# Performance work log

Hardware: AMD Instinct MI355X
Metric: run time of the kernel (lower is better)

The kernel has to match this reference:

```python
import jax, jax.numpy as jnp
import numpy as np

NMS_THRESH = 0.5
SCORE_THRESH = 0.2
MAX_SUBJECT = 15
MAX_OBJECT = 15
B, NS, NO = 32, 512, 512


def _make_boxes(k, b, n):
    u = jax.random.uniform(k, (b, n, 4))
    xy = u[..., :2] * 1000.0          # top-left corner
    wh = u[..., 2:] * 200.0 + 1.0     # positive width/height
    return jnp.concatenate([xy, xy + wh], axis=-1)  # valid xyxy boxes


def setup_inputs() -> dict:
    key = jax.random.key(0)
    ks = jax.random.split(key, 6)
    return {
        "subj_boxes": _make_boxes(ks[0], B, NS),
        "subj_scores": jax.random.uniform(ks[1], (B, NS)),
        "subj_labels": jax.random.randint(ks[2], (B, NS), 0, 30, dtype=jnp.int32),
        "obj_boxes": _make_boxes(ks[3], B, NO),
        "obj_scores": jax.random.uniform(ks[4], (B, NO)),
        "obj_labels": jax.random.randint(ks[5], (B, NO), 0, 30, dtype=jnp.int32),
    }


def reference(subj_boxes, subj_scores, subj_labels, obj_boxes, obj_scores, obj_labels):
    # concat subject + object detections per image, as in preprocess()
    boxes = jnp.concatenate([subj_boxes, obj_boxes], axis=1)    # [B,N,4]
    scores = jnp.concatenate([subj_scores, obj_scores], axis=1) # [B,N]
    labels = jnp.concatenate([subj_labels, obj_labels], axis=1) # [B,N]
    b, n = scores.shape
    is_subj = jnp.arange(n) < subj_boxes.shape[1]               # [N]

    # sort by score descending (matches the argsort after NMS; greedy NMS
    # preserves this ordering among survivors)
    order = jnp.argsort(-scores, axis=1)
    boxes = jnp.take_along_axis(boxes, order[..., None], axis=1)
    scores = jnp.take_along_axis(scores, order, axis=1)
    labels = jnp.take_along_axis(labels, order, axis=1)
    is_subj = jnp.take(is_subj, order)                          # [B,N]

    active = scores >= SCORE_THRESH

    # torchvision batched_nms: offset boxes per class so distinct classes
    # never overlap (comparisons only -> no gradient path)
    max_coord = jax.lax.stop_gradient(jnp.max(boxes))
    ob = boxes + labels.astype(boxes.dtype)[..., None] * (max_coord + 1.0)

    # pairwise IoU [B,N,N]
    area = (ob[..., 2] - ob[..., 0]) * (ob[..., 3] - ob[..., 1])
    lt = jnp.maximum(ob[:, :, None, :2], ob[:, None, :, :2])
    rb = jnp.minimum(ob[:, :, None, 2:], ob[:, None, :, 2:])
    wh = jnp.clip(rb - lt, 0.0)
    inter = wh[..., 0] * wh[..., 1]
    iou = inter / (area[:, :, None] + area[:, None, :] - inter)

    later = jnp.arange(n)[None, :] > jnp.arange(n)[:, None]     # strictly lower-score

    def body(i, suppressed):  # greedy NMS, vectorized over batch
        keep_i = active[:, i] & ~suppressed[:, i]
        return suppressed | (keep_i[:, None] & (iou[:, i, :] > NMS_THRESH) & later[i])

    suppressed = jax.lax.fori_loop(0, n, body, jnp.zeros((b, n), dtype=bool))
    kept = active & ~suppressed

    # split survivors into subjects / objects, keep top max_subject/max_object
    neg = jnp.finfo(scores.dtype).min
    sub_key = jnp.where(kept & is_subj, scores, neg)
    obj_key = jnp.where(kept & ~is_subj, scores, neg)
    sv, si = jax.lax.top_k(sub_key, MAX_SUBJECT)
    ov, oi = jax.lax.top_k(obj_key, MAX_OBJECT)
    idx = jnp.concatenate([si, oi], axis=1)                     # [B,K]
    valid = jnp.concatenate([sv, ov], axis=1) > neg             # [B,K]

    out_boxes = jnp.take_along_axis(boxes, idx[..., None], axis=1) * valid[..., None]
    out_scores = jnp.take_along_axis(scores, idx, axis=1) * valid
    out_labels = jnp.where(valid, jnp.take_along_axis(labels, idx, axis=1), -1)
    num_subjects = jnp.sum(sv > neg, axis=1)
    return out_boxes, out_scores, out_labels, num_subjects, valid
```

## Files before the change

### kernel.cpp

```cpp
#include <hip/hip_runtime.h>
#include <stdint.h>

#define BQ    32
#define NSUB  512
#define NDET  1024
#define NCLS  30
#define KSLOT 30
#define BCAP  96

#pragma clang fp contract(off)

typedef unsigned long long u64;

__global__ __launch_bounds__(512) void bucket_kernel(
    const float* __restrict__ sb, const float* __restrict__ ss,
    const int*   __restrict__ sl,
    const float* __restrict__ ob, const float* __restrict__ os,
    const int*   __restrict__ ol,
    float* __restrict__ pmax, int* __restrict__ cnts,
    u64* __restrict__ bkeys)
{
    const int b    = blockIdx.x;
    const int t    = threadIdx.x;
    const int lane = t & 63;
    const int w    = t >> 6;

    __shared__ int   lcnt[NCLS];
    __shared__ u64   lkey[NCLS][BCAP];
    __shared__ float wred[8];

    if (t < NCLS) lcnt[t] = 0;

    const float4* s4 = (const float4*)(sb + (size_t)b * NSUB * 4);
    const float4* o4 = (const float4*)(ob + (size_t)b * NSUB * 4);
    float4 a = s4[t], c4 = o4[t];
    float m = fmaxf(fmaxf(fmaxf(a.x, a.y), fmaxf(a.z, a.w)),
                    fmaxf(fmaxf(c4.x, c4.y), fmaxf(c4.z, c4.w)));
    for (int off = 32; off; off >>= 1) m = fmaxf(m, __shfl_xor(m, off));
    if (lane == 0) wred[w] = m;
    __syncthreads();
    if (t == 0) {
        float mm = wred[0];
        for (int i = 1; i < 8; ++i) mm = fmaxf(mm, wred[i]);
        pmax[b] = mm;
    }

    {
        float sc = ss[b * NSUB + t];
        int   lb = sl[b * NSUB + t];
        if (sc >= 0.2f) {
            int pos = atomicAdd(&lcnt[lb], 1);
            if (pos < BCAP)
                lkey[lb][pos] = ((u64)__float_as_uint(sc) << 32) | (u64)(1023 - t);
        }
    }
    {
        float sc = os[b * NSUB + t];
        int   lb = ol[b * NSUB + t];
        if (sc >= 0.2f) {
            int pos = atomicAdd(&lcnt[lb], 1);
            if (pos < BCAP)
                lkey[lb][pos] = ((u64)__float_as_uint(sc) << 32) | (u64)(1023 - (512 + t));
        }
    }
    __syncthreads();

    if (t < NCLS) {
        int c = lcnt[t];
        cnts[b * NCLS + t] = (c < BCAP) ? c : BCAP;
    }
    for (int s = t; s < NCLS * BCAP; s += 512) {
        int c = s / BCAP, k = s - c * BCAP;
        if (k < lcnt[c])
            bkeys[((size_t)b * NCLS + c) * BCAP + k] = lkey[c][k];
    }
}

__global__ __launch_bounds__(64) void nms_class_kernel(
    const float* __restrict__ sb, const float* __restrict__ ob,
    const float* __restrict__ pmax, const int* __restrict__ cnts,
    const u64* __restrict__ bkeys,
    u64* __restrict__ subk, u64* __restrict__ objk)
{
#pragma clang fp contract(off)
    const int c    = blockIdx.x;
    const int b    = blockIdx.y;
    const int lane = threadIdx.x;

    __shared__ u64    keyarr[BCAP];
    __shared__ u64    skey[BCAP];
    __shared__ float4 bx4[BCAP];

    float pv = pmax[lane & 31];
    for (int off = 32; off; off >>= 1) pv = fmaxf(pv, __shfl_xor(pv, off));
    const float mco  = pv + 1.0f;
    const float offc = (float)c * mco;

    int cnt = cnts[b * NCLS + c];
    const u64* src = bkeys + ((size_t)b * NCLS + c) * BCAP;
    if (lane < cnt)        keyarr[lane]      = src[lane];
    if (64 + lane < cnt)   keyarr[64 + lane] = src[64 + lane];
    __syncthreads();

    {
        u64 K = (lane < cnt) ? keyarr[lane] : 0;
        int r = 0;
        for (int l = 0; l < cnt; ++l) r += (keyarr[l] > K) ? 1 : 0;
        if (lane < cnt) skey[r] = K;
    }
    if (cnt > 64) {
        int e = 64 + lane;
        u64 K = (e < cnt) ? keyarr[e] : 0;
        int r = 0;
        for (int l = 0; l < cnt; ++l) r += (keyarr[l] > K) ? 1 : 0;
        if (e < cnt) skey[r] = K;
    }
    __syncthreads();

    const int  lim1  = (cnt < 64) ? cnt : 64;
    const bool have1 = (lane < lim1);
    u64 SK1 = have1 ? skey[lane] : 0;
    int idx1 = 1023 - (int)(unsigned)(SK1 & 0xffffffffull);
    float4 bj1 = make_float4(0.f, 0.f, 0.f, 0.f);
    if (have1) {
        bj1 = (idx1 < NSUB)
            ? *(const float4*)(sb + (size_t)(b * NSUB + idx1) * 4)
            : *(const float4*)(ob + (size_t)(b * NSUB + idx1 - NSUB) * 4);
        bx4[lane] = bj1;
    }
    const bool have2 = (64 + lane) < cnt;
    u64 SK2 = 0; int idx2 = 0; float4 bj2 = make_float4(0.f, 0.f, 0.f, 0.f);
    if (cnt > 64) {
        SK2 = have2 ? skey[64 + lane] : 0;
        idx2 = 1023 - (int)(unsigned)(SK2 & 0xffffffffull);
        if (have2) {
            bj2 = (idx2 < NSUB)
                ? *(const float4*)(sb + (size_t)(b * NSUB + idx2) * 4)
                : *(const float4*)(ob + (size_t)(b * NSUB + idx2 - NSUB) * 4);
            bx4[64 + lane] = bj2;
        }
    }
    __syncthreads();

    float j0 = bj1.x + offc, j1 = bj1.y + offc;
    float j2v = bj1.z + offc, j3 = bj1.w + offc;
    float aj = (j2v - j0) * (j3 - j1);
    u64 ov = 0;
    for (int l = 0; l < lim1; ++l) {
        float4 bl = bx4[l];
        float i0 = bl.x + offc, i1 = bl.y + offc;
        float i2 = bl.z + offc, i3 = bl.w + offc;
        float ai = (i2 - i0) * (i3 - i1);
        if (have1 && l < lane) {
            float ltx = fmaxf(i0, j0), lty = fmaxf(i1, j1);
            float rbx = fminf(i2, j2v), rby = fminf(i3, j3);
            float wx = fmaxf(rbx - ltx, 0.0f), wy = fmaxf(rby - lty, 0.0f);
            float inter = wx * wy;
            float iou = inter / ((ai + aj) - inter);
            if (iou > 0.5f) ov |= (1ull << l);
        }
    }
    bool sup1 = !have1;
    for (int l = 0; l < lim1; ++l) {
        u64 bal = __ballot(sup1);
        if (!((bal >> l) & 1ull)) sup1 = sup1 || (((ov >> l) & 1ull) != 0ull);
    }
    const bool kept1 = have1 && !sup1;
    const u64 keptA = __ballot(kept1);

    bool kept2 = false;
    if (cnt > 64) {
        float k0 = bj2.x + offc, k1 = bj2.y + offc;
        float k2 = bj2.z + offc, k3 = bj2.w + offc;
        float ak = (k2 - k0) * (k3 - k1);
        bool sup2 = !have2;
        for (int l = 0; l < 64; ++l) {
            if ((keptA >> l) & 1ull) {
                float4 bl = bx4[l];
                float i0 = bl.x + offc, i1 = bl.y + offc;
                float i2 = bl.z + offc, i3 = bl.w + offc;
                float ai = (i2 - i0) * (i3 - i1);
                if (!sup2) {
                    float ltx = fmaxf(i0, k0), lty = fmaxf(i1, k1);
                    float rbx = fminf(i2, k2), rby = fminf(i3, k3);
                    float wx = fmaxf(rbx - ltx, 0.0f), wy = fmaxf(rby - lty, 0.0f);
                    float inter = wx * wy;
                    float iou = inter / ((ai + ak) - inter);
                    if (iou > 0.5f) sup2 = true;
                }
            }
        }
        u64 ov2 = 0;
        const int lim2 = cnt - 64;
        for (int l = 0; l < lim2; ++l) {
            float4 bl = bx4[64 + l];
            float i0 = bl.x + offc, i1 = bl.y + offc;
            float i2 = bl.z + offc, i3 = bl.w + offc;
            float ai = (i2 - i0) * (i3 - i1);
            if (have2 && l < lane) {
                float ltx = fmaxf(i0, k0), lty = fmaxf(i1, k1);
                float rbx = fminf(i2, k2), rby = fminf(i3, k3);
                float wx = fmaxf(rbx - ltx, 0.0f), wy = fmaxf(rby - lty, 0.0f);
                float inter = wx * wy;
                float iou = inter / ((ai + ak) - inter);
                if (iou > 0.5f) ov2 |= (1ull << l);
            }
        }
        for (int l = 0; l < lim2; ++l) {
            u64 bal = __ballot(sup2);
            if (!((bal >> l) & 1ull)) sup2 = sup2 || (((ov2 >> l) & 1ull) != 0ull);
        }
        kept2 = have2 && !sup2;
    }

    const bool s1 = kept1 && (idx1 < NSUB), o1 = kept1 && (idx1 >= NSUB);
    const bool s2 = kept2 && (idx2 < NSUB), o2 = kept2 && (idx2 >= NSUB);
    const u64 mS1 = __ballot(s1), mS2 = __ballot(s2);
    const u64 mO1 = __ballot(o1), mO2 = __ballot(o2);
    const u64 ltm = (1ull << lane) - 1ull;
    u64* subp = subk + ((size_t)b * NCLS + c) * 15;
    u64* objp = objk + ((size_t)b * NCLS + c) * 15;
    if (s1) { int p = (int)__popcll(mS1 & ltm); if (p < 15) subp[p] = SK1; }
    if (s2) { int p = (int)__popcll(mS1) + (int)__popcll(mS2 & ltm); if (p < 15) subp[p] = SK2; }
    if (o1) { int p = (int)__popcll(mO1 & ltm); if (p < 15) objp[p] = SK1; }
    if (o2) { int p = (int)__popcll(mO1) + (int)__popcll(mO2 & ltm); if (p < 15) objp[p] = SK2; }
    int tS = (int)(__popcll(mS1) + __popcll(mS2)); if (tS > 15) tS = 15;
    int tO = (int)(__popcll(mO1) + __popcll(mO2)); if (tO > 15) tO = 15;
    if (lane >= tS && lane < 15) subp[lane] = 0;
    if (lane >= tO && lane < 15) objp[lane] = 0;
}

__global__ __launch_bounds__(64) void select_kernel(
    const float* __restrict__ sb, const int* __restrict__ sl,
    const float* __restrict__ ob, const int* __restrict__ ol,
    const u64* __restrict__ subk, const u64* __restrict__ objk,
    float* __restrict__ out)
{
    const int b    = blockIdx.x;
    const int side = blockIdx.y;
    const int lane = threadIdx.x;

    float* outB = out;
    float* outS = out + BQ * KSLOT * 4;
    float* outL = outS + BQ * KSLOT;
    float* outN = outL + BQ * KSLOT;
    float* outV = outN + BQ;

    const u64* src = (side ? objk : subk) + (size_t)b * NCLS * 15;
    u64 kk[8];
    #pragma unroll
    for (int i = 0; i < 8; ++i) {
        int p = lane + 64 * i;
        kk[i] = (p < NCLS * 15) ? src[p] : 0;
    }
    int nvalid = 0;
    for (int r = 0; r < 15; ++r) {
        u64 lm = 0; int li = 0;
        #pragma unroll
        for (int i = 0; i < 8; ++i) if (kk[i] > lm) { lm = kk[i]; li = i; }
        u64 gm = lm;
        for (int off = 32; off; off >>= 1) {
            u64 o = __shfl_xor(gm, off);
            if (o > gm) gm = o;
        }
        int p = b * KSLOT + (side ? (15 + r) : r);
        if (gm == 0) {
            if (lane == 0) {
                *(float4*)(outB + (size_t)p * 4) = make_float4(0.f, 0.f, 0.f, 0.f);
                outS[p] = 0.0f; outL[p] = -1.0f; outV[p] = 0.0f;
            }
        } else {
            u64 win = __ballot(lm == gm);
            int wl = (int)__ffsll(win) - 1;
            if (lane == wl) {
                kk[li] = 0;
                int idx = 1023 - (int)(unsigned)(gm & 0xffffffffull);
                float score = __uint_as_float((unsigned)(gm >> 32));
                float4 bx; int lb;
                if (idx < NSUB) {
                    bx = *(const float4*)(sb + (size_t)(b * NSUB + idx) * 4);
                    lb = sl[b * NSUB + idx];
                } else {
                    bx = *(const float4*)(ob + (size_t)(b * NSUB + idx - NSUB) * 4);
                    lb = ol[b * NSUB + idx - NSUB];
                }
                *(float4*)(outB + (size_t)p * 4) = bx;
                outS[p] = score;
                outL[p] = (float)lb;
                outV[p] = 1.0f;
            }
            nvalid++;
        }
    }
    if (side == 0 && lane == 0) outN[b] = (float)nvalid;
}

extern "C" void kernel_launch(void* const* d_in, const int* in_sizes, int n_in,
                              void* d_out, int out_size, void* d_ws, size_t ws_size,
                              hipStream_t stream) {
    const float* sb = (const float*)d_in[0];
    const float* ss = (const float*)d_in[1];
    const int*   sl = (const int*)d_in[2];
    const float* ob = (const float*)d_in[3];
    const float* os = (const float*)d_in[4];
    const int*   ol = (const int*)d_in[5];

    float* pmax  = (float*)d_ws;
    int*   cnts  = (int*)((char*)d_ws + 256);
    u64*   bkeys = (u64*)((char*)d_ws + 8192);
    u64*   subk  = bkeys + (size_t)BQ * NCLS * BCAP;
    u64*   objk  = subk + (size_t)BQ * NCLS * 15;

    bucket_kernel<<<dim3(BQ), dim3(512), 0, stream>>>(
        sb, ss, sl, ob, os, ol, pmax, cnts, bkeys);
    nms_class_kernel<<<dim3(NCLS, BQ), dim3(64), 0, stream>>>(
        sb, ob, pmax, cnts, bkeys, subk, objk);
    select_kernel<<<dim3(BQ, 2), dim3(64), 0, stream>>>(
        sb, sl, ob, ol, subk, objk, (float*)d_out);
}
```

Measured before the change: 89.99 us.

## Fuse bucketing, per-class NMS and top-k selection into one per-image kernel

Three kernels become two: a small global-max kernel, then a single 1024-thread block per image. That block buckets detections by class in shared memory, runs per-class NMS with one wavefront per class (two classes for some waves), and does the subject/object top-15 selection from shared-memory candidate lists. This removes two launches and the workspace round-trips for bucket keys and per-class candidates, and box/label lookups now come from shared memory instead of global gathers. The cost is less parallelism: 32 blocks instead of 960 wave-sized blocks. The per-class work is serialized within waves, and the large shared-memory footprint limits occupancy.

```diff
diff --git a/kernel.cpp b/kernel.cpp
--- a/kernel.cpp
+++ b/kernel.cpp
@@ -12,233 +12,199 @@
 
 typedef unsigned long long u64;
 
-__global__ __launch_bounds__(512) void bucket_kernel(
+__global__ __launch_bounds__(512) void max_kernel(
+    const float4* __restrict__ sb4, const float4* __restrict__ ob4,
+    float* __restrict__ pmax)
+{
+    const int b = blockIdx.x, t = threadIdx.x;
+    __shared__ float wred[8];
+    float4 a  = sb4[(size_t)b * NSUB + t];
+    float4 c4 = ob4[(size_t)b * NSUB + t];
+    float m = fmaxf(fmaxf(fmaxf(a.x, a.y), fmaxf(a.z, a.w)),
+                    fmaxf(fmaxf(c4.x, c4.y), fmaxf(c4.z, c4.w)));
+    for (int off = 32; off; off >>= 1) m = fmaxf(m, __shfl_xor(m, off));
+    if ((t & 63) == 0) wred[t >> 6] = m;
+    __syncthreads();
+    if (t == 0) {
+        float mm = wred[0];
+        for (int i = 1; i < 8; ++i) mm = fmaxf(mm, wred[i]);
+        pmax[b] = mm;
+    }
+}
+
+__global__ __launch_bounds__(1024) void nms_fused_kernel(
     const float* __restrict__ sb, const float* __restrict__ ss,
     const int*   __restrict__ sl,
     const float* __restrict__ ob, const float* __restrict__ os,
     const int*   __restrict__ ol,
-    float* __restrict__ pmax, int* __restrict__ cnts,
-    u64* __restrict__ bkeys)
+    const float* __restrict__ pmax,
+    float* __restrict__ out)
 {
+#pragma clang fp contract(off)
     const int b    = blockIdx.x;
     const int t    = threadIdx.x;
     const int lane = t & 63;
     const int w    = t >> 6;
 
-    __shared__ int   lcnt[NCLS];
-    __shared__ u64   lkey[NCLS][BCAP];
-    __shared__ float wred[8];
+    __shared__ int    lcnt[NCLS];
+    __shared__ u64    lkey[NCLS][BCAP];
+    __shared__ u64    skeyw[16][BCAP];
+    __shared__ float4 bxw[16][BCAP];
+    __shared__ float4 lbox[NDET];
+    __shared__ int    llab[NDET];
+    __shared__ u64    subcand[512];
+    __shared__ u64    objcand[512];
+
+    float pv = pmax[lane & 31];
+    for (int off = 32; off; off >>= 1) pv = fmaxf(pv, __shfl_xor(pv, off));
+    const float mco = pv + 1.0f;
 
     if (t < NCLS) lcnt[t] = 0;
-
-    const float4* s4 = (const float4*)(sb + (size_t)b * NSUB * 4);
-    const float4* o4 = (const float4*)(ob + (size_t)b * NSUB * 4);
-    float4 a = s4[t], c4 = o4[t];
-    float m = fmaxf(fmaxf(fmaxf(a.x, a.y), fmaxf(a.z, a.w)),
-                    fmaxf(fmaxf(c4.x, c4.y), fmaxf(c4.z, c4.w)));
-    for (int off = 32; off; off >>= 1) m = fmaxf(m, __shfl_xor(m, off));
-    if (lane == 0) wred[w] = m;
-    __syncthreads();
-    if (t == 0) {
-        float mm = wred[0];
-        for (int i = 1; i < 8; ++i) mm = fmaxf(mm, wred[i]);
-        pmax[b] = mm;
-    }
+    if (t < 512) { subcand[t] = 0; objcand[t] = 0; }
+    __syncthreads();
 
     {
-        float sc = ss[b * NSUB + t];
-        int   lb = sl[b * NSUB + t];
+        float sc; int lb; float4 bx;
+        if (t < NSUB) {
+            sc = ss[b * NSUB + t];  lb = sl[b * NSUB + t];
+            bx = *(const float4*)(sb + (size_t)(b * NSUB + t) * 4);
+        } else {
+            int u = t - NSUB;
+            sc = os[b * NSUB + u];  lb = ol[b * NSUB + u];
+            bx = *(const float4*)(ob + (size_t)(b * NSUB + u) * 4);
+        }
+        lbox[t] = bx;
+        llab[t] = lb;
         if (sc >= 0.2f) {
             int pos = atomicAdd(&lcnt[lb], 1);
             if (pos < BCAP)
                 lkey[lb][pos] = ((u64)__float_as_uint(sc) << 32) | (u64)(1023 - t);
         }
     }
-    {
-        float sc = os[b * NSUB + t];
-        int   lb = ol[b * NSUB + t];
-        if (sc >= 0.2f) {
-            int pos = atomicAdd(&lcnt[lb], 1);
-            if (pos < BCAP)
-                lkey[lb][pos] = ((u64)__float_as_uint(sc) << 32) | (u64)(1023 - (512 + t));
-        }
-    }
-    __syncthreads();
-
-    if (t < NCLS) {
-        int c = lcnt[t];
-        cnts[b * NCLS + t] = (c < BCAP) ? c : BCAP;
-    }
-    for (int s = t; s < NCLS * BCAP; s += 512) {
-        int c = s / BCAP, k = s - c * BCAP;
-        if (k < lcnt[c])
-            bkeys[((size_t)b * NCLS + c) * BCAP + k] = lkey[c][k];
-    }
-}
-
-__global__ __launch_bounds__(64) void nms_class_kernel(
-    const float* __restrict__ sb, const float* __restrict__ ob,
-    const float* __restrict__ pmax, const int* __restrict__ cnts,
-    const u64* __restrict__ bkeys,
-    u64* __restrict__ subk, u64* __restrict__ objk)
-{
-#pragma clang fp contract(off)
-    const int c    = blockIdx.x;
-    const int b    = blockIdx.y;
-    const int lane = threadIdx.x;
-
-    __shared__ u64    keyarr[BCAP];
-    __shared__ u64    skey[BCAP];
-    __shared__ float4 bx4[BCAP];
-
-    float pv = pmax[lane & 31];
-    for (int off = 32; off; off >>= 1) pv = fmaxf(pv, __shfl_xor(pv, off));
-    const float mco  = pv + 1.0f;
-    const float offc = (float)c * mco;
-
-    int cnt = cnts[b * NCLS + c];
-    const u64* src = bkeys + ((size_t)b * NCLS + c) * BCAP;
-    if (lane < cnt)        keyarr[lane]      = src[lane];
-    if (64 + lane < cnt)   keyarr[64 + lane] = src[64 + lane];
-    __syncthreads();
-
-    {
-        u64 K = (lane < cnt) ? keyarr[lane] : 0;
-        int r = 0;
-        for (int l = 0; l < cnt; ++l) r += (keyarr[l] > K) ? 1 : 0;
-        if (lane < cnt) skey[r] = K;
-    }
-    if (cnt > 64) {
-        int e = 64 + lane;
-        u64 K = (e < cnt) ? keyarr[e] : 0;
-        int r = 0;
-        for (int l = 0; l < cnt; ++l) r += (keyarr[l] > K) ? 1 : 0;
-        if (e < cnt) skey[r] = K;
-    }
-    __syncthreads();
-
-    const int  lim1  = (cnt < 64) ? cnt : 64;
-    const bool have1 = (lane < lim1);
-    u64 SK1 = have1 ? skey[lane] : 0;
-    int idx1 = 1023 - (int)(unsigned)(SK1 & 0xffffffffull);
-    float4 bj1 = make_float4(0.f, 0.f, 0.f, 0.f);
-    if (have1) {
-        bj1 = (idx1 < NSUB)
-            ? *(const float4*)(sb + (size_t)(b * NSUB + idx1) * 4)
-            : *(const float4*)(ob + (size_t)(b * NSUB + idx1 - NSUB) * 4);
-        bx4[lane] = bj1;
-    }
-    const bool have2 = (64 + lane) < cnt;
-    u64 SK2 = 0; int idx2 = 0; float4 bj2 = make_float4(0.f, 0.f, 0.f, 0.f);
-    if (cnt > 64) {
-        SK2 = have2 ? skey[64 + lane] : 0;
-        idx2 = 1023 - (int)(unsigned)(SK2 & 0xffffffffull);
-        if (have2) {
-            bj2 = (idx2 < NSUB)
-                ? *(const float4*)(sb + (size_t)(b * NSUB + idx2) * 4)
-                : *(const float4*)(ob + (size_t)(b * NSUB + idx2 - NSUB) * 4);
-            bx4[64 + lane] = bj2;
-        }
-    }
-    __syncthreads();
-
-    float j0 = bj1.x + offc, j1 = bj1.y + offc;
-    float j2v = bj1.z + offc, j3 = bj1.w + offc;
-    float aj = (j2v - j0) * (j3 - j1);
-    u64 ov = 0;
-    for (int l = 0; l < lim1; ++l) {
-        float4 bl = bx4[l];
-        float i0 = bl.x + offc, i1 = bl.y + offc;
-        float i2 = bl.z + offc, i3 = bl.w + offc;
-        float ai = (i2 - i0) * (i3 - i1);
-        if (have1 && l < lane) {
-            float ltx = fmaxf(i0, j0), lty = fmaxf(i1, j1);
-            float rbx = fminf(i2, j2v), rby = fminf(i3, j3);
-            float wx = fmaxf(rbx - ltx, 0.0f), wy = fmaxf(rby - lty, 0.0f);
-            float inter = wx * wy;
-            float iou = inter / ((ai + aj) - inter);
-            if (iou > 0.5f) ov |= (1ull << l);
-        }
-    }
-    bool sup1 = !have1;
-    for (int l = 0; l < lim1; ++l) {
-        u64 bal = __ballot(sup1);
-        if (!((bal >> l) & 1ull)) sup1 = sup1 || (((ov >> l) & 1ull) != 0ull);
-    }
-    const bool kept1 = have1 && !sup1;
-    const u64 keptA = __ballot(kept1);
-
-    bool kept2 = false;
-    if (cnt > 64) {
-        float k0 = bj2.x + offc, k1 = bj2.y + offc;
-        float k2 = bj2.z + offc, k3 = bj2.w + offc;
-        float ak = (k2 - k0) * (k3 - k1);
-        bool sup2 = !have2;
-        for (int l = 0; l < 64; ++l) {
-            if ((keptA >> l) & 1ull) {
-                float4 bl = bx4[l];
+    __syncthreads();
+
+    for (int ci = 0; ci < 2; ++ci) {
+        const int c = w + 16 * ci;
+        if (c >= NCLS) break;
+        int cnt = lcnt[c]; if (cnt > BCAP) cnt = BCAP;
+        const float offc = (float)c * mco;
+        u64*    SKY = skeyw[w];
+        float4* BX  = bxw[w];
+
+        {
+            u64 K = (lane < cnt) ? lkey[c][lane] : 0;
+            int r = 0;
+            for (int l = 0; l < cnt; ++l) r += (lkey[c][l] > K) ? 1 : 0;
+            if (lane < cnt) SKY[r] = K;
+        }
+        if (cnt > 64) {
+            int e = 64 + lane;
+            u64 K = (e < cnt) ? lkey[c][e] : 0;
+            int r = 0;
+            for (int l = 0; l < cnt; ++l) r += (lkey[c][l] > K) ? 1 : 0;
+            if (e < cnt) SKY[r] = K;
+        }
+        __threadfence_block();
+
+        const int  lim1  = (cnt < 64) ? cnt : 64;
+        const bool have1 = (lane < lim1);
+        u64 SK1 = have1 ? SKY[lane] : 0;
+        int idx1 = 1023 - (int)(unsigned)(SK1 & 0xffffffffull);
+        float4 bj1 = make_float4(0.f, 0.f, 0.f, 0.f);
+        if (have1) { bj1 = lbox[idx1]; BX[lane] = bj1; }
+        const bool have2 = (64 + lane) < cnt;
+        u64 SK2 = 0; int idx2 = 0; float4 bj2 = make_float4(0.f, 0.f, 0.f, 0.f);
+        if (cnt > 64) {
+            SK2 = have2 ? SKY[64 + lane] : 0;
+            idx2 = 1023 - (int)(unsigned)(SK2 & 0xffffffffull);
+            if (have2) { bj2 = lbox[idx2]; BX[64 + lane] = bj2; }
+        }
+        __threadfence_block();
+
+        float j0 = bj1.x + offc, j1 = bj1.y + offc;
+        float j2v = bj1.z + offc, j3 = bj1.w + offc;
+        float aj = (j2v - j0) * (j3 - j1);
+        u64 ov = 0;
+        for (int l = 0; l < lim1; ++l) {
+            float4 bl = BX[l];
+            float i0 = bl.x + offc, i1 = bl.y + offc;
+            float i2 = bl.z + offc, i3 = bl.w + offc;
+            float ai = (i2 - i0) * (i3 - i1);
+            if (have1 && l < lane) {
+                float ltx = fmaxf(i0, j0), lty = fmaxf(i1, j1);
+                float rbx = fminf(i2, j2v), rby = fminf(i3, j3);
+                float wx = fmaxf(rbx - ltx, 0.0f), wy = fmaxf(rby - lty, 0.0f);
+                float inter = wx * wy;
+                float iou = inter / ((ai + aj) - inter);
+                if (iou > 0.5f) ov |= (1ull << l);
+            }
+        }
+        bool sup1 = !have1;
+        for (int l = 0; l < lim1; ++l) {
+            u64 bal = __ballot(sup1);
+            if (!((bal >> l) & 1ull)) sup1 = sup1 || (((ov >> l) & 1ull) != 0ull);
+        }
+        const bool kept1 = have1 && !sup1;
+        const u64 keptA = __ballot(kept1);
+
+        bool kept2 = false;
+        if (cnt > 64) {
+            float k0 = bj2.x + offc, k1 = bj2.y + offc;
+            float k2 = bj2.z + offc, k3 = bj2.w + offc;
+            float ak = (k2 - k0) * (k3 - k1);
+            bool sup2 = !have2;
+            for (int l = 0; l < 64; ++l) {
+                if ((keptA >> l) & 1ull) {
+                    float4 bl = BX[l];
+                    float i0 = bl.x + offc, i1 = bl.y + offc;
+                    float i2 = bl.z + offc, i3 = bl.w + offc;
+                    float ai = (i2 - i0) * (i3 - i1);
+                    if (!sup2) {
+                        float ltx = fmaxf(i0, k0), lty = fmaxf(i1, k1);
+                        float rbx = fminf(i2, k2), rby = fminf(i3, k3);
+                        float wx = fmaxf(rbx - ltx, 0.0f), wy = fmaxf(rby - lty, 0.0f);
+                        float inter = wx * wy;
+                        float iou = inter / ((ai + ak) - inter);
+                        if (iou > 0.5f) sup2 = true;
+                    }
+                }
+            }
+            u64 ov2 = 0;
+            const int lim2 = cnt - 64;
+            for (int l = 0; l < lim2; ++l) {
+                float4 bl = BX[64 + l];
                 float i0 = bl.x + offc, i1 = bl.y + offc;
                 float i2 = bl.z + offc, i3 = bl.w + offc;
                 float ai = (i2 - i0) * (i3 - i1);
-                if (!sup2) {
+                if (have2 && l < lane) {
                     float ltx = fmaxf(i0, k0), lty = fmaxf(i1, k1);
                     float rbx = fminf(i2, k2), rby = fminf(i3, k3);
                     float wx = fmaxf(rbx - ltx, 0.0f), wy = fmaxf(rby - lty, 0.0f);
                     float inter = wx * wy;
                     float iou = inter / ((ai + ak) - inter);
-                    if (iou > 0.5f) sup2 = true;
-                }
-            }
-        }
-        u64 ov2 = 0;
-        const int lim2 = cnt - 64;
-        for (int l = 0; l < lim2; ++l) {
-            float4 bl = bx4[64 + l];
-            float i0 = bl.x + offc, i1 = bl.y + offc;
-            float i2 = bl.z + offc, i3 = bl.w + offc;
-            float ai = (i2 - i0) * (i3 - i1);
-            if (have2 && l < lane) {
-                float ltx = fmaxf(i0, k0), lty = fmaxf(i1, k1);
-                float rbx = fminf(i2, k2), rby = fminf(i3, k3);
-                float wx = fmaxf(rbx - ltx, 0.0f), wy = fmaxf(rby - lty, 0.0f);
-                float inter = wx * wy;
-                float iou = inter / ((ai + ak) - inter);
-                if (iou > 0.5f) ov2 |= (1ull << l);
-            }
-        }
-        for (int l = 0; l < lim2; ++l) {
-            u64 bal = __ballot(sup2);
-            if (!((bal >> l) & 1ull)) sup2 = sup2 || (((ov2 >> l) & 1ull) != 0ull);
-        }
-        kept2 = have2 && !sup2;
-    }
-
-    const bool s1 = kept1 && (idx1 < NSUB), o1 = kept1 && (idx1 >= NSUB);
-    const bool s2 = kept2 && (idx2 < NSUB), o2 = kept2 && (idx2 >= NSUB);
-    const u64 mS1 = __ballot(s1), mS2 = __ballot(s2);
-    const u64 mO1 = __ballot(o1), mO2 = __ballot(o2);
-    const u64 ltm = (1ull << lane) - 1ull;
-    u64* subp = subk + ((size_t)b * NCLS + c) * 15;
-    u64* objp = objk + ((size_t)b * NCLS + c) * 15;
-    if (s1) { int p = (int)__popcll(mS1 & ltm); if (p < 15) subp[p] = SK1; }
-    if (s2) { int p = (int)__popcll(mS1) + (int)__popcll(mS2 & ltm); if (p < 15) subp[p] = SK2; }
-    if (o1) { int p = (int)__popcll(mO1 & ltm); if (p < 15) objp[p] = SK1; }
-    if (o2) { int p = (int)__popcll(mO1) + (int)__popcll(mO2 & ltm); if (p < 15) objp[p] = SK2; }
-    int tS = (int)(__popcll(mS1) + __popcll(mS2)); if (tS > 15) tS = 15;
-    int tO = (int)(__popcll(mO1) + __popcll(mO2)); if (tO > 15) tO = 15;
-    if (lane >= tS && lane < 15) subp[lane] = 0;
-    if (lane >= tO && lane < 15) objp[lane] = 0;
-}
-
-__global__ __launch_bounds__(64) void select_kernel(
-    const float* __restrict__ sb, const int* __restrict__ sl,
-    const float* __restrict__ ob, const int* __restrict__ ol,
-    const u64* __restrict__ subk, const u64* __restrict__ objk,
-    float* __restrict__ out)
-{
-    const int b    = blockIdx.x;
-    const int side = blockIdx.y;
-    const int lane = threadIdx.x;
+                    if (iou > 0.5f) ov2 |= (1ull << l);
+                }
+            }
+            for (int l = 0; l < lim2; ++l) {
+                u64 bal = __ballot(sup2);
+                if (!((bal >> l) & 1ull)) sup2 = sup2 || (((ov2 >> l) & 1ull) != 0ull);
+            }
+            kept2 = have2 && !sup2;
+        }
+
+        const bool s1 = kept1 && (idx1 < NSUB), o1 = kept1 && (idx1 >= NSUB);
+        const bool s2 = kept2 && (idx2 < NSUB), o2 = kept2 && (idx2 >= NSUB);
+        const u64 mS1 = __ballot(s1), mS2 = __ballot(s2);
+        const u64 mO1 = __ballot(o1), mO2 = __ballot(o2);
+        const u64 ltm = (1ull << lane) - 1ull;
+        u64* subp = subcand + c * 15;
+        u64* objp = objcand + c * 15;
+        if (s1) { int p = (int)__popcll(mS1 & ltm); if (p < 15) subp[p] = SK1; }
+        if (s2) { int p = (int)__popcll(mS1) + (int)__popcll(mS2 & ltm); if (p < 15) subp[p] = SK2; }
+        if (o1) { int p = (int)__popcll(mO1 & ltm); if (p < 15) objp[p] = SK1; }
+        if (o2) { int p = (int)__popcll(mO1) + (int)__popcll(mO2 & ltm); if (p < 15) objp[p] = SK2; }
+    }
+    __syncthreads();
 
     float* outB = out;
     float* outS = out + BQ * KSLOT * 4;
@@ -246,53 +212,48 @@
     float* outN = outL + BQ * KSLOT;
     float* outV = outN + BQ;
 
-    const u64* src = (side ? objk : subk) + (size_t)b * NCLS * 15;
-    u64 kk[8];
-    #pragma unroll
-    for (int i = 0; i < 8; ++i) {
-        int p = lane + 64 * i;
-        kk[i] = (p < NCLS * 15) ? src[p] : 0;
-    }
-    int nvalid = 0;
-    for (int r = 0; r < 15; ++r) {
-        u64 lm = 0; int li = 0;
+    if (w < 2) {
+        const int side = w;
+        const u64* src = side ? objcand : subcand;
+        u64 kk[8];
         #pragma unroll
-        for (int i = 0; i < 8; ++i) if (kk[i] > lm) { lm = kk[i]; li = i; }
-        u64 gm = lm;
-        for (int off = 32; off; off >>= 1) {
-            u64 o = __shfl_xor(gm, off);
-            if (o > gm) gm = o;
-        }
-        int p = b * KSLOT + (side ? (15 + r) : r);
-        if (gm == 0) {
-            if (lane == 0) {
-                *(float4*)(outB + (size_t)p * 4) = make_float4(0.f, 0.f, 0.f, 0.f);
-                outS[p] = 0.0f; outL[p] = -1.0f; outV[p] = 0.0f;
-            }
-        } else {
-            u64 win = __ballot(lm == gm);
-            int wl = (int)__ffsll(win) - 1;
-            if (lane == wl) {
-                kk[li] = 0;
-                int idx = 1023 - (int)(unsigned)(gm & 0xffffffffull);
-                float score = __uint_as_float((unsigned)(gm >> 32));
-                float4 bx; int lb;
-                if (idx < NSUB) {
-                    bx = *(const float4*)(sb + (size_t)(b * NSUB + idx) * 4);
-                    lb = sl[b * NSUB + idx];
-                } else {
-                    bx = *(const float4*)(ob + (size_t)(b * NSUB + idx - NSUB) * 4);
-                    lb = ol[b * NSUB + idx - NSUB];
-                }
-                *(float4*)(outB + (size_t)p * 4) = bx;
-                outS[p] = score;
-                outL[p] = (float)lb;
-                outV[p] = 1.0f;
-            }
-            nvalid++;
-        }
-    }
-    if (side == 0 && lane == 0) outN[b] = (float)nvalid;
+        for (int i = 0; i < 8; ++i) {
+            int p = lane + 64 * i;
+            kk[i] = (p < NCLS * 15) ? src[p] : 0;
+        }
+        int nvalid = 0;
+        for (int r = 0; r < 15; ++r) {
+            u64 lm = 0; int li = 0;
+            #pragma unroll
+            for (int i = 0; i < 8; ++i) if (kk[i] > lm) { lm = kk[i]; li = i; }
+            u64 gm = lm;
+            for (int off = 32; off; off >>= 1) {
+                u64 o = __shfl_xor(gm, off);
+                if (o > gm) gm = o;
+            }
+            int p = b * KSLOT + (side ? (15 + r) : r);
+            if (gm == 0) {
+                if (lane == 0) {
+                    *(float4*)(outB + (size_t)p * 4) = make_float4(0.f, 0.f, 0.f, 0.f);
+                    outS[p] = 0.0f; outL[p] = -1.0f; outV[p] = 0.0f;
+                }
+            } else {
+                u64 win = __ballot(lm == gm);
+                int wl = (int)__ffsll(win) - 1;
+                if (lane == wl) {
+                    kk[li] = 0;
+                    int idx = 1023 - (int)(unsigned)(gm & 0xffffffffull);
+                    float score = __uint_as_float((unsigned)(gm >> 32));
+                    *(float4*)(outB + (size_t)p * 4) = lbox[idx];
+                    outS[p] = score;
+                    outL[p] = (float)llab[idx];
+                    outV[p] = 1.0f;
+                }
+                nvalid++;
+            }
+        }
+        if (side == 0 && lane == 0) outN[b] = (float)nvalid;
+    }
 }
 
 extern "C" void kernel_launch(void* const* d_in, const int* in_sizes, int n_in,
@@ -305,16 +266,10 @@
     const float* os = (const float*)d_in[4];
     const int*   ol = (const int*)d_in[5];
 
-    float* pmax  = (float*)d_ws;
-    int*   cnts  = (int*)((char*)d_ws + 256);
-    u64*   bkeys = (u64*)((char*)d_ws + 8192);
-    u64*   subk  = bkeys + (size_t)BQ * NCLS * BCAP;
-    u64*   objk  = subk + (size_t)BQ * NCLS * 15;
-
-    bucket_kernel<<<dim3(BQ), dim3(512), 0, stream>>>(
-        sb, ss, sl, ob, os, ol, pmax, cnts, bkeys);
-    nms_class_kernel<<<dim3(NCLS, BQ), dim3(64), 0, stream>>>(
-        sb, ob, pmax, cnts, bkeys, subk, objk);
-    select_kernel<<<dim3(BQ, 2), dim3(64), 0, stream>>>(
-        sb, sl, ob, ol, subk, objk, (float*)d_out);
+    float* pmax = (float*)d_ws;
+
+    max_kernel<<<dim3(BQ), dim3(512), 0, stream>>>(
+        (const float4*)sb, (const float4*)ob, pmax);
+    nms_fused_kernel<<<dim3(BQ), dim3(1024), 0, stream>>>(
+        sb, ss, sl, ob, os, ol, pmax, (float*)d_out);
 }
```

Result: slower. 102.1 us (+13.4%).

## Scatter boxes with keys in bucket pass and drop LDS staging and syncs

Applied to the files above, without the earlier changes.

The bucket kernel now writes each detection's key and box directly to global per-class buckets, with no staging through a shared-memory array and no copy-out loop. The NMS kernel reads boxes alongside keys, carries them through the rank sort into shared memory, and no longer gathers them from the original inputs. It also issues the global loads unconditionally up front and replaces __syncthreads with __threadfence_block, since each block is a single wavefront. The goal is to remove the dependent gather latency and the barriers, at the cost of more workspace traffic and a reliance on single-wave ordering.

```diff
diff --git a/kernel.cpp b/kernel.cpp
--- a/kernel.cpp
+++ b/kernel.cpp
@@ -18,24 +18,22 @@
     const float* __restrict__ ob, const float* __restrict__ os,
     const int*   __restrict__ ol,
     float* __restrict__ pmax, int* __restrict__ cnts,
-    u64* __restrict__ bkeys)
+    u64* __restrict__ bkeys, float4* __restrict__ bboxes)
 {
-    const int b    = blockIdx.x;
-    const int t    = threadIdx.x;
-    const int lane = t & 63;
-    const int w    = t >> 6;
-
+    const int b = blockIdx.x, t = threadIdx.x;
+    const int lane = t & 63, w = t >> 6;
     __shared__ int   lcnt[NCLS];
-    __shared__ u64   lkey[NCLS][BCAP];
     __shared__ float wred[8];
 
     if (t < NCLS) lcnt[t] = 0;
 
-    const float4* s4 = (const float4*)(sb + (size_t)b * NSUB * 4);
-    const float4* o4 = (const float4*)(ob + (size_t)b * NSUB * 4);
-    float4 a = s4[t], c4 = o4[t];
-    float m = fmaxf(fmaxf(fmaxf(a.x, a.y), fmaxf(a.z, a.w)),
-                    fmaxf(fmaxf(c4.x, c4.y), fmaxf(c4.z, c4.w)));
+    float4 bxs = *(const float4*)(sb + (size_t)(b * NSUB + t) * 4);
+    float4 bxo = *(const float4*)(ob + (size_t)(b * NSUB + t) * 4);
+    float scs = ss[b * NSUB + t];  int lbs = sl[b * NSUB + t];
+    float sco = os[b * NSUB + t];  int lbo = ol[b * NSUB + t];
+
+    float m = fmaxf(fmaxf(fmaxf(bxs.x, bxs.y), fmaxf(bxs.z, bxs.w)),
+                    fmaxf(fmaxf(bxo.x, bxo.y), fmaxf(bxo.z, bxo.w)));
     for (int off = 32; off; off >>= 1) m = fmaxf(m, __shfl_xor(m, off));
     if (lane == 0) wred[w] = m;
     __syncthreads();
@@ -45,41 +43,32 @@
         pmax[b] = mm;
     }
 
-    {
-        float sc = ss[b * NSUB + t];
-        int   lb = sl[b * NSUB + t];
-        if (sc >= 0.2f) {
-            int pos = atomicAdd(&lcnt[lb], 1);
-            if (pos < BCAP)
-                lkey[lb][pos] = ((u64)__float_as_uint(sc) << 32) | (u64)(1023 - t);
-        }
-    }
-    {
-        float sc = os[b * NSUB + t];
-        int   lb = ol[b * NSUB + t];
-        if (sc >= 0.2f) {
-            int pos = atomicAdd(&lcnt[lb], 1);
-            if (pos < BCAP)
-                lkey[lb][pos] = ((u64)__float_as_uint(sc) << 32) | (u64)(1023 - (512 + t));
+    if (scs >= 0.2f) {
+        int pos = atomicAdd(&lcnt[lbs], 1);
+        if (pos < BCAP) {
+            size_t s = ((size_t)b * NCLS + lbs) * BCAP + pos;
+            bkeys[s]  = ((u64)__float_as_uint(scs) << 32) | (u64)(1023 - t);
+            bboxes[s] = bxs;
+        }
+    }
+    if (sco >= 0.2f) {
+        int pos = atomicAdd(&lcnt[lbo], 1);
+        if (pos < BCAP) {
+            size_t s = ((size_t)b * NCLS + lbo) * BCAP + pos;
+            bkeys[s]  = ((u64)__float_as_uint(sco) << 32) | (u64)(1023 - (512 + t));
+            bboxes[s] = bxo;
         }
     }
     __syncthreads();
-
     if (t < NCLS) {
         int c = lcnt[t];
         cnts[b * NCLS + t] = (c < BCAP) ? c : BCAP;
     }
-    for (int s = t; s < NCLS * BCAP; s += 512) {
-        int c = s / BCAP, k = s - c * BCAP;
-        if (k < lcnt[c])
-            bkeys[((size_t)b * NCLS + c) * BCAP + k] = lkey[c][k];
-    }
 }
 
 __global__ __launch_bounds__(64) void nms_class_kernel(
-    const float* __restrict__ sb, const float* __restrict__ ob,
     const float* __restrict__ pmax, const int* __restrict__ cnts,
-    const u64* __restrict__ bkeys,
+    const u64* __restrict__ bkeys, const float4* __restrict__ bboxes,
     u64* __restrict__ subk, u64* __restrict__ objk)
 {
 #pragma clang fp contract(off)
@@ -89,65 +78,59 @@
 
     __shared__ u64    keyarr[BCAP];
     __shared__ u64    skey[BCAP];
-    __shared__ float4 bx4[BCAP];
-
+    __shared__ float4 bxs4[BCAP];
+
+    const size_t base = (size_t)b * NCLS + c;
+
+    u64    K1 = bkeys[base * BCAP + lane];
+    float4 B1 = bboxes[base * BCAP + lane];
+    u64 K2 = 0; float4 B2 = make_float4(0.f, 0.f, 0.f, 0.f);
+    if (lane < BCAP - 64) {
+        K2 = bkeys[base * BCAP + 64 + lane];
+        B2 = bboxes[base * BCAP + 64 + lane];
+    }
+    const int cnt = cnts[base];
     float pv = pmax[lane & 31];
     for (int off = 32; off; off >>= 1) pv = fmaxf(pv, __shfl_xor(pv, off));
     const float mco  = pv + 1.0f;
     const float offc = (float)c * mco;
 
-    int cnt = cnts[b * NCLS + c];
-    const u64* src = bkeys + ((size_t)b * NCLS + c) * BCAP;
-    if (lane < cnt)        keyarr[lane]      = src[lane];
-    if (64 + lane < cnt)   keyarr[64 + lane] = src[64 + lane];
-    __syncthreads();
+    keyarr[lane] = K1;
+    if (lane < BCAP - 64) keyarr[64 + lane] = K2;
+    __threadfence_block();
 
     {
-        u64 K = (lane < cnt) ? keyarr[lane] : 0;
         int r = 0;
-        for (int l = 0; l < cnt; ++l) r += (keyarr[l] > K) ? 1 : 0;
-        if (lane < cnt) skey[r] = K;
+        for (int l = 0; l < cnt; ++l) r += (keyarr[l] > K1) ? 1 : 0;
+        if (lane < cnt) { skey[r] = K1; bxs4[r] = B1; }
     }
     if (cnt > 64) {
         int e = 64 + lane;
-        u64 K = (e < cnt) ? keyarr[e] : 0;
         int r = 0;
-        for (int l = 0; l < cnt; ++l) r += (keyarr[l] > K) ? 1 : 0;
-        if (e < cnt) skey[r] = K;
-    }
-    __syncthreads();
+        for (int l = 0; l < cnt; ++l) r += (keyarr[l] > K2) ? 1 : 0;
+        if (e < cnt) { skey[r] = K2; bxs4[r] = B2; }
+    }
+    __threadfence_block();
 
     const int  lim1  = (cnt < 64) ? cnt : 64;
     const bool have1 = (lane < lim1);
     u64 SK1 = have1 ? skey[lane] : 0;
     int idx1 = 1023 - (int)(unsigned)(SK1 & 0xffffffffull);
-    float4 bj1 = make_float4(0.f, 0.f, 0.f, 0.f);
-    if (have1) {
-        bj1 = (idx1 < NSUB)
-            ? *(const float4*)(sb + (size_t)(b * NSUB + idx1) * 4)
-            : *(const float4*)(ob + (size_t)(b * NSUB + idx1 - NSUB) * 4);
-        bx4[lane] = bj1;
-    }
+    float4 bj1 = have1 ? bxs4[lane] : make_float4(0.f, 0.f, 0.f, 0.f);
     const bool have2 = (64 + lane) < cnt;
     u64 SK2 = 0; int idx2 = 0; float4 bj2 = make_float4(0.f, 0.f, 0.f, 0.f);
     if (cnt > 64) {
         SK2 = have2 ? skey[64 + lane] : 0;
         idx2 = 1023 - (int)(unsigned)(SK2 & 0xffffffffull);
-        if (have2) {
-            bj2 = (idx2 < NSUB)
-                ? *(const float4*)(sb + (size_t)(b * NSUB + idx2) * 4)
-                : *(const float4*)(ob + (size_t)(b * NSUB + idx2 - NSUB) * 4);
-            bx4[64 + lane] = bj2;
-        }
-    }
-    __syncthreads();
+        if (have2) bj2 = bxs4[64 + lane];
+    }
 
     float j0 = bj1.x + offc, j1 = bj1.y + offc;
     float j2v = bj1.z + offc, j3 = bj1.w + offc;
     float aj = (j2v - j0) * (j3 - j1);
     u64 ov = 0;
     for (int l = 0; l < lim1; ++l) {
-        float4 bl = bx4[l];
+        float4 bl = bxs4[l];
         float i0 = bl.x + offc, i1 = bl.y + offc;
         float i2 = bl.z + offc, i3 = bl.w + offc;
         float ai = (i2 - i0) * (i3 - i1);
@@ -176,7 +159,7 @@
         bool sup2 = !have2;
         for (int l = 0; l < 64; ++l) {
             if ((keptA >> l) & 1ull) {
-                float4 bl = bx4[l];
+                float4 bl = bxs4[l];
                 float i0 = bl.x + offc, i1 = bl.y + offc;
                 float i2 = bl.z + offc, i3 = bl.w + offc;
                 float ai = (i2 - i0) * (i3 - i1);
@@ -193,7 +176,7 @@
         u64 ov2 = 0;
         const int lim2 = cnt - 64;
         for (int l = 0; l < lim2; ++l) {
-            float4 bl = bx4[64 + l];
+            float4 bl = bxs4[64 + l];
             float i0 = bl.x + offc, i1 = bl.y + offc;
             float i2 = bl.z + offc, i3 = bl.w + offc;
             float ai = (i2 - i0) * (i3 - i1);
@@ -218,8 +201,8 @@
     const u64 mS1 = __ballot(s1), mS2 = __ballot(s2);
     const u64 mO1 = __ballot(o1), mO2 = __ballot(o2);
     const u64 ltm = (1ull << lane) - 1ull;
-    u64* subp = subk + ((size_t)b * NCLS + c) * 15;
-    u64* objp = objk + ((size_t)b * NCLS + c) * 15;
+    u64* subp = subk + base * 15;
+    u64* objp = objk + base * 15;
     if (s1) { int p = (int)__popcll(mS1 & ltm); if (p < 15) subp[p] = SK1; }
     if (s2) { int p = (int)__popcll(mS1) + (int)__popcll(mS2 & ltm); if (p < 15) subp[p] = SK2; }
     if (o1) { int p = (int)__popcll(mO1 & ltm); if (p < 15) objp[p] = SK1; }
@@ -305,16 +288,17 @@
     const float* os = (const float*)d_in[4];
     const int*   ol = (const int*)d_in[5];
 
-    float* pmax  = (float*)d_ws;
-    int*   cnts  = (int*)((char*)d_ws + 256);
-    u64*   bkeys = (u64*)((char*)d_ws + 8192);
-    u64*   subk  = bkeys + (size_t)BQ * NCLS * BCAP;
-    u64*   objk  = subk + (size_t)BQ * NCLS * 15;
+    float*  pmax   = (float*)d_ws;
+    int*    cnts   = (int*)((char*)d_ws + 256);
+    u64*    bkeys  = (u64*)((char*)d_ws + 8192);
+    float4* bboxes = (float4*)((char*)d_ws + 745472);
+    u64*    subk   = (u64*)((char*)d_ws + 2220032);
+    u64*    objk   = subk + (size_t)BQ * NCLS * 15;
 
     bucket_kernel<<<dim3(BQ), dim3(512), 0, stream>>>(
-        sb, ss, sl, ob, os, ol, pmax, cnts, bkeys);
+        sb, ss, sl, ob, os, ol, pmax, cnts, bkeys, bboxes);
     nms_class_kernel<<<dim3(NCLS, BQ), dim3(64), 0, stream>>>(
-        sb, ob, pmax, cnts, bkeys, subk, objk);
+        pmax, cnts, bkeys, bboxes, subk, objk);
     select_kernel<<<dim3(BQ, 2), dim3(64), 0, stream>>>(
         sb, sl, ob, ol, subk, objk, (float*)d_out);
 }
```

New measurement: 87.72 us (median of 2 runs). -2.5%, faster.
